# Optimization experiments

Measured on AMD Instinct MI355X. Metric: run time of the kernel, lower is better.

Reference implementation:

```python
import jax, jax.numpy as jnp
import numpy as np

DIM = 768
HEADS = 12
DIM_HEAD = 64
INNER = HEADS * DIM_HEAD  # 768
SCALE = DIM_HEAD ** -0.5


def setup_inputs() -> dict:
    key = jax.random.key(0)
    k1, k2, k3, k4 = jax.random.split(key, 4)
    b, n = 8, 1024
    x = jax.random.normal(k1, (b, n, DIM), dtype=jnp.float32)
    # fused QKV projection, no bias: y = x @ w_qkv  -> [b, n, 3*inner]
    w_qkv = jax.random.normal(k2, (DIM, 3 * INNER), dtype=jnp.float32) * (DIM ** -0.5)
    # output projection with bias
    w_out = jax.random.normal(k3, (INNER, DIM), dtype=jnp.float32) * (INNER ** -0.5)
    b_out = jax.random.normal(k4, (DIM,), dtype=jnp.float32) * 0.02
    return {"x": x, "w_qkv": w_qkv, "w_out": w_out, "b_out": b_out}


def reference(x, w_qkv, w_out, b_out):
    b, n, _ = x.shape
    qkv = jnp.einsum('bnd,de->bne', x, w_qkv)  # [b, n, 3*inner]
    q, k, v = jnp.split(qkv, 3, axis=-1)
    # 'b n (h d) -> b h n d'
    def split_heads(t):
        return t.reshape(b, n, HEADS, DIM_HEAD).transpose(0, 2, 1, 3)
    q, k, v = split_heads(q), split_heads(k), split_heads(v)
    dots = jnp.einsum('bhid,bhjd->bhij', q, k) * SCALE  # [b, h, n, n]
    attn = jax.nn.softmax(dots, axis=-1)
    out = jnp.einsum('bhij,bhjd->bhid', attn, v)  # [b, h, n, d]
    out = out.transpose(0, 2, 1, 3).reshape(b, n, INNER)  # 'b h n d -> b n (h d)'
    return jnp.einsum('bne,ed->bnd', out, w_out) + b_out
```

## Files before the change

### kernel.cpp

```cpp
#include <hip/hip_runtime.h>

typedef unsigned short u16;
typedef __bf16 bf16x8 __attribute__((ext_vector_type(8)));
typedef float f32x4 __attribute__((ext_vector_type(4)));

__device__ inline u16 f2bf(float f) {
    union { float f; unsigned int u; } a; a.f = f;
    unsigned int u = a.u + 0x7fffu + ((a.u >> 16) & 1u);
    return (u16)(u >> 16);
}
__device__ __forceinline__ float truncbf(float f, u16& h) {
    union { float f; unsigned int u; } a; a.f = f;
    a.u &= 0xffff0000u;
    h = (u16)(a.u >> 16);
    return a.f;
}

__device__ __forceinline__ void cp16(const void* g, void* l) {
    __builtin_amdgcn_global_load_lds(
        (const __attribute__((address_space(1))) unsigned int*)g,
        (__attribute__((address_space(3))) unsigned int*)l, 16, 0, 0);
}

__global__ __launch_bounds__(256) void prep(
    const float* __restrict__ x, const float* __restrict__ wq,
    const float* __restrict__ wo, u16* __restrict__ xbf,
    u16* __restrict__ wtq, u16* __restrict__ wto)
{
    int bid = blockIdx.x;
    if (bid < 3072) {
        size_t base = ((size_t)bid * 256 + threadIdx.x) * 8;
        float4 f0 = *(const float4*)&x[base];
        float4 f1 = *(const float4*)&x[base + 4];
        union { u16 s[8]; uint4 v; } t;
        t.s[0]=f2bf(f0.x); t.s[1]=f2bf(f0.y); t.s[2]=f2bf(f0.z); t.s[3]=f2bf(f0.w);
        t.s[4]=f2bf(f1.x); t.s[5]=f2bf(f1.y); t.s[6]=f2bf(f1.z); t.s[7]=f2bf(f1.w);
        *(uint4*)&xbf[base] = t.v;
        return;
    }
    __shared__ u16 tile[32][33];
    const float* in; u16* outp; int N, bx, by;
    if (bid < 3072 + 1728) { int t = bid - 3072; in = wq; outp = wtq; N = 2304; bx = t % 72; by = t / 72; }
    else                   { int t = bid - 4800; in = wo; outp = wto; N = 768;  bx = t % 24; by = t / 24; }
    int n0 = bx * 32, k0 = by * 32;
    int tx = threadIdx.x & 31, ty = threadIdx.x >> 5;
    #pragma unroll
    for (int r = ty; r < 32; r += 8)
        tile[r][tx] = f2bf(in[(size_t)(k0 + r) * N + n0 + tx]);
    __syncthreads();
    #pragma unroll
    for (int r = ty; r < 32; r += 8)
        outp[(size_t)(n0 + r) * 768 + k0 + tx] = tile[tx][r];
}

__global__ __launch_bounds__(256) void gemm_qkv(
    const u16* __restrict__ A, const u16* __restrict__ Bt,
    u16* __restrict__ q_out, u16* __restrict__ k_out, u16* __restrict__ v_out)
{
    const int K = 768;
    __shared__ __align__(16) u16 As[128 * 64];
    __shared__ __align__(16) u16 Bs[128 * 64];

    int tid = threadIdx.x;
    int lane = tid & 63, wave = tid >> 6;
    int quad = lane >> 4, l16 = lane & 15;
    int wm = wave >> 1, wn = wave & 1;
    int id = blockIdx.x;
    int xcd = id & 7, j = id >> 3;
    int m0 = (((j & 7) << 3) + xcd) * 128;
    int n0 = (j >> 3) * 128;

    f32x4 acc[4][4];
    #pragma unroll
    for (int i = 0; i < 4; i++)
        #pragma unroll
        for (int jj = 0; jj < 4; jj++) acc[i][jj] = (f32x4){0.f, 0.f, 0.f, 0.f};

    int r0 = tid >> 3, cg = tid & 7;
    for (int kt = 0; kt < K; kt += 64) {
        #pragma unroll
        for (int it = 0; it < 4; ++it) {
            int row = it * 32 + r0;
            int g = cg ^ (row & 7);
            cp16(&A [(size_t)(m0 + row) * K + kt + g * 8], &As[(size_t)(it * 256 + tid) * 8]);
            cp16(&Bt[(size_t)(n0 + row) * K + kt + g * 8], &Bs[(size_t)(it * 256 + tid) * 8]);
        }
        __syncthreads();
        #pragma unroll
        for (int ko = 0; ko < 2; ko++) {
            bf16x8 af[4], bfr[4];
            #pragma unroll
            for (int i = 0; i < 4; i++) {
                int R = wm * 64 + i * 16 + l16;
                af[i] = *(const bf16x8*)&As[R * 64 + (((ko * 4 + quad) ^ (R & 7)) * 8)];
            }
            #pragma unroll
            for (int jj = 0; jj < 4; jj++) {
                int R = wn * 64 + jj * 16 + l16;
                bfr[jj] = *(const bf16x8*)&Bs[R * 64 + (((ko * 4 + quad) ^ (R & 7)) * 8)];
            }
            #pragma unroll
            for (int i = 0; i < 4; i++)
                #pragma unroll
                for (int jj = 0; jj < 4; jj++)
                    acc[i][jj] = __builtin_amdgcn_mfma_f32_16x16x32_bf16(af[i], bfr[jj], acc[i][jj], 0, 0, 0);
        }
        __syncthreads();
    }

    int M0 = m0 + wm * 64, N0 = n0 + wn * 64;
    int part = N0 >= 1536 ? 2 : (N0 >= 768 ? 1 : 0);
    int h = (N0 - part * 768) >> 6;
    int b = M0 >> 10, npos0 = M0 & 1023;
    u16* ep = (wave < 2 ? As : Bs) + (wave & 1) * 4096;

    if (part != 2) {
        float scale = (part == 0) ? 0.18033688011112042f : 1.0f;
        u16* gbase = (part == 0 ? q_out : k_out) + (((size_t)(b * 12 + h) * 1024 + npos0) << 6);
        #pragma unroll
        for (int i = 0; i < 4; i++)
            #pragma unroll
            for (int jj = 0; jj < 4; jj++) {
                int dd = jj * 16 + l16;
                #pragma unroll
                for (int r = 0; r < 4; r++) {
                    int np = i * 16 + quad * 4 + r;
                    ep[np * 64 + (((dd >> 3) ^ (np & 7)) * 8) + (dd & 7)] =
                        f2bf(acc[i][jj][r] * scale);
                }
            }
        __syncthreads();
        #pragma unroll
        for (int t = 0; t < 8; t++) {
            int idx = t * 512 + lane * 8;
            int np = idx >> 6;
            int slot = ((lane & 7) ^ (np & 7));
            uint4 v = *(const uint4*)&ep[np * 64 + slot * 8];
            *(uint4*)&gbase[idx] = v;
        }
    } else {
        #pragma unroll
        for (int i = 0; i < 4; i++)
            #pragma unroll
            for (int jj = 0; jj < 4; jj++) {
                int dd = jj * 16 + l16;
                int npg = i * 2 + (quad >> 1);
                int sub = (quad & 1) * 4;
                union { u16 s[4]; uint2 v; } pk;
                #pragma unroll
                for (int r = 0; r < 4; r++) pk.s[r] = f2bf(acc[i][jj][r]);
                *(uint2*)&ep[dd * 64 + ((npg ^ (dd & 7)) * 8) + sub] = pk.v;
            }
        __syncthreads();
        #pragma unroll
        for (int t = 0; t < 8; t++) {
            int dd = t * 8 + (lane >> 3);
            int npg = lane & 7;
            uint4 v = *(const uint4*)&ep[dd * 64 + ((npg ^ (dd & 7)) * 8)];
            *(uint4*)&v_out[((size_t)((b * 12 + h) * 64 + dd)) * 1024 + npos0 + npg * 8] = v;
        }
    }
}

__global__ __launch_bounds__(256) void attn128(
    u16* __restrict__ QO, const u16* __restrict__ Kg, const u16* __restrict__ Vtg)
{
    __shared__ __align__(16) u16 Ks[64 * 64];
    __shared__ __align__(16) u16 Vs[64 * 64];

    int tid = threadIdx.x;
    int lane = tid & 63, wave = tid >> 6;
    int quad = lane >> 4, l16 = lane & 15;
    int id = blockIdx.x;
    int xcd = id & 7, j = id >> 3;
    int bh = xcd * 12 + (j >> 3);
    int q0 = (j & 7) * 128;
    const size_t head_base = (size_t)bh * 65536;

    size_t qoff[2];
    bf16x8 qf[2][2];
    #pragma unroll
    for (int qs = 0; qs < 2; qs++) {
        qoff[qs] = head_base + (size_t)(q0 + wave * 32 + qs * 16 + l16) * 64;
        qf[qs][0] = *(const bf16x8*)&QO[qoff[qs] + quad * 8];
        qf[qs][1] = *(const bf16x8*)&QO[qoff[qs] + 32 + quad * 8];
    }

    f32x4 Oacc[4][2];
    #pragma unroll
    for (int dt = 0; dt < 4; dt++)
        #pragma unroll
        for (int qs = 0; qs < 2; qs++) Oacc[dt][qs] = (f32x4){0.f, 0.f, 0.f, 0.f};
    float l_part[2] = {0.f, 0.f};

    int srow = tid >> 3, sg = tid & 7;
    for (int j0 = 0; j0 < 1024; j0 += 64) {
        #pragma unroll
        for (int it = 0; it < 2; ++it) {
            int e = it * 256 + tid, row = it * 32 + srow, gs = sg ^ (row & 7);
            cp16(&Kg [head_base + (size_t)(j0 + row) * 64 + gs * 8], &Ks[(size_t)e * 8]);
            cp16(&Vtg[head_base + (size_t)row * 1024 + j0 + gs * 8], &Vs[(size_t)e * 8]);
        }
        __syncthreads();

        f32x4 s4[4][2];
        #pragma unroll
        for (int nt = 0; nt < 4; nt++) {
            int R = nt * 16 + l16;
            bf16x8 kf0 = *(const bf16x8*)&Ks[R * 64 + ((quad       ^ (R & 7)) * 8)];
            bf16x8 kf1 = *(const bf16x8*)&Ks[R * 64 + (((quad + 4) ^ (R & 7)) * 8)];
            #pragma unroll
            for (int qs = 0; qs < 2; qs++) {
                f32x4 s = (f32x4){0.f, 0.f, 0.f, 0.f};
                s = __builtin_amdgcn_mfma_f32_16x16x32_bf16(kf0, qf[qs][0], s, 0, 0, 0);
                s = __builtin_amdgcn_mfma_f32_16x16x32_bf16(kf1, qf[qs][1], s, 0, 0, 0);
                s4[nt][qs] = s;
            }
        }

        u16 ph[4][2][4];
        #pragma unroll
        for (int nt = 0; nt < 4; nt++)
            #pragma unroll
            for (int qs = 0; qs < 2; qs++)
                #pragma unroll
                for (int r = 0; r < 4; r++) {
                    float p = __builtin_amdgcn_exp2f(s4[nt][qs][r]);
                    l_part[qs] += truncbf(p, ph[nt][qs][r]);
                }

        #pragma unroll
        for (int h = 0; h < 2; h++) {
            union { u16 s[8]; bf16x8 v; } pk[2];
            #pragma unroll
            for (int qs = 0; qs < 2; qs++)
                #pragma unroll
                for (int r = 0; r < 4; r++) {
                    pk[qs].s[r]     = ph[2 * h][qs][r];
                    pk[qs].s[4 + r] = ph[2 * h + 1][qs][r];
                }
            int lg0 = 4 * h + (quad >> 1), lg1 = lg0 + 2;
            int off = (quad & 1) * 4;
            #pragma unroll
            for (int dt = 0; dt < 4; dt++) {
                int drow = dt * 16 + l16;
                union { u16 s[8]; bf16x8 v; } vk;
                *(uint2*)&vk.s[0] = *(const uint2*)&Vs[drow * 64 + (lg0 ^ (drow & 7)) * 8 + off];
                *(uint2*)&vk.s[4] = *(const uint2*)&Vs[drow * 64 + (lg1 ^ (drow & 7)) * 8 + off];
                #pragma unroll
                for (int qs = 0; qs < 2; qs++)
                    Oacc[dt][qs] = __builtin_amdgcn_mfma_f32_16x16x32_bf16(vk.v, pk[qs].v, Oacc[dt][qs], 0, 0, 0);
            }
        }
        __syncthreads();
    }

    #pragma unroll
    for (int qs = 0; qs < 2; qs++) {
        float l = l_part[qs];
        l += __shfl_xor(l, 16);
        l += __shfl_xor(l, 32);
        float rl = __builtin_amdgcn_rcpf(l);
        #pragma unroll
        for (int dt = 0; dt < 4; dt++) {
            union { u16 s[4]; uint2 v; } ok;
            #pragma unroll
            for (int r = 0; r < 4; r++) ok.s[r] = f2bf(Oacc[dt][qs][r] * rl);
            *(uint2*)&QO[qoff[qs] + dt * 16 + quad * 4] = ok.v;
        }
    }
}

__global__ __launch_bounds__(256) void gemm_out(
    const u16* __restrict__ Qg, const u16* __restrict__ Bt,
    const float* __restrict__ bias, float* __restrict__ out)
{
    const int K = 768;
    __shared__ __align__(16) u16 As[128 * 64];
    __shared__ __align__(16) u16 Bs[128 * 64];

    int tid = threadIdx.x;
    int lane = tid & 63, wave = tid >> 6;
    int quad = lane >> 4, l16 = lane & 15;
    int wm = wave >> 1, wn = wave & 1;
    int id = blockIdx.x;
    int xcd = id & 7, j = id >> 3;
    int m0 = (((j & 7) << 3) + xcd) * 128;
    int n0 = (j >> 3) * 128;

    f32x4 acc[4][4];
    #pragma unroll
    for (int i = 0; i < 4; i++)
        #pragma unroll
        for (int jj = 0; jj < 4; jj++) acc[i][jj] = (f32x4){0.f, 0.f, 0.f, 0.f};

    int r0 = tid >> 3, cg = tid & 7;
    for (int kt = 0; kt < K; kt += 64) {
        int h = kt >> 6;
        #pragma unroll
        for (int it = 0; it < 4; ++it) {
            int row = it * 32 + r0;
            int g = cg ^ (row & 7);
            int m = m0 + row, b = m >> 10, npos = m & 1023;
            cp16(&Qg[(((size_t)(b * 12 + h) * 1024 + npos) << 6) + g * 8],
                 &As[(size_t)(it * 256 + tid) * 8]);
            cp16(&Bt[(size_t)(n0 + row) * K + kt + g * 8],
                 &Bs[(size_t)(it * 256 + tid) * 8]);
        }
        __syncthreads();
        #pragma unroll
        for (int ko = 0; ko < 2; ko++) {
            bf16x8 af[4], bfr[4];
            #pragma unroll
            for (int i = 0; i < 4; i++) {
                int R = wm * 64 + i * 16 + l16;
                af[i] = *(const bf16x8*)&As[R * 64 + (((ko * 4 + quad) ^ (R & 7)) * 8)];
            }
            #pragma unroll
            for (int jj = 0; jj < 4; jj++) {
                int R = wn * 64 + jj * 16 + l16;
                bfr[jj] = *(const bf16x8*)&Bs[R * 64 + (((ko * 4 + quad) ^ (R & 7)) * 8)];
            }
            #pragma unroll
            for (int i = 0; i < 4; i++)
                #pragma unroll
                for (int jj = 0; jj < 4; jj++)
                    acc[i][jj] = __builtin_amdgcn_mfma_f32_16x16x32_bf16(af[i], bfr[jj], acc[i][jj], 0, 0, 0);
        }
        __syncthreads();
    }

    #pragma unroll
    for (int i = 0; i < 4; i++) {
        int mbase = m0 + wm * 64 + i * 16 + quad * 4;
        #pragma unroll
        for (int jj = 0; jj < 4; jj++) {
            int n = n0 + wn * 64 + jj * 16 + l16;
            float bv = bias[n];
            #pragma unroll
            for (int r = 0; r < 4; r++)
                out[(size_t)(mbase + r) * 768 + n] = acc[i][jj][r] + bv;
        }
    }
}

extern "C" void kernel_launch(void* const* d_in, const int* in_sizes, int n_in,
                              void* d_out, int out_size, void* d_ws, size_t ws_size,
                              hipStream_t stream) {
    const float* x     = (const float*)d_in[0];
    const float* w_qkv = (const float*)d_in[1];
    const float* w_out = (const float*)d_in[2];
    const float* b_out = (const float*)d_in[3];
    float* out = (float*)d_out;

    char* ws = (char*)d_ws;
    u16* wtq  = (u16*)(ws);
    u16* wto  = (u16*)(ws + 3538944);
    u16* Qbuf = (u16*)(ws + 4718592);
    u16* xbf  = (u16*)(ws + 17301504);
    u16* Kbuf = (u16*)d_out;
    u16* Vbuf = (u16*)d_out + 6291456;

    prep<<<dim3(5376), 256, 0, stream>>>(x, w_qkv, w_out, xbf, wtq, wto);
    gemm_qkv<<<dim3(1152), 256, 0, stream>>>(xbf, wtq, Qbuf, Kbuf, Vbuf);
    attn128<<<dim3(768), 256, 0, stream>>>(Qbuf, Kbuf, Vbuf);
    gemm_out<<<dim3(384), 256, 0, stream>>>(Qbuf, wto, b_out, out);
}
```

Measured before the change: 194.3 us.

## Double-buffer LDS tiles with async prefetch in GEMM and attention kernels

All three main kernels (QKV GEMM, attention, output GEMM) now keep two LDS buffers. Each iteration issues async global-to-LDS loads for the next K/V or K-tile into the other buffer while it runs MFMAs on the current one. Fragments are read into registers before the prefetch is issued, which lets each loop drop to a single barrier per iteration. Global address pointers are precomputed outside the loops, and the redundant epilogue barriers in the QKV GEMM are removed. The cost is doubled LDS use per block, which may lower occupancy, plus more registers for the held fragments.

```diff
diff --git a/kernel.cpp b/kernel.cpp
--- a/kernel.cpp
+++ b/kernel.cpp
@@ -58,8 +58,8 @@
     u16* __restrict__ q_out, u16* __restrict__ k_out, u16* __restrict__ v_out)
 {
     const int K = 768;
-    __shared__ __align__(16) u16 As[128 * 64];
-    __shared__ __align__(16) u16 Bs[128 * 64];
+    __shared__ __align__(16) u16 As[2][128 * 64];
+    __shared__ __align__(16) u16 Bs[2][128 * 64];
 
     int tid = threadIdx.x;
     int lane = tid & 63, wave = tid >> 6;
@@ -77,46 +77,55 @@
         for (int jj = 0; jj < 4; jj++) acc[i][jj] = (f32x4){0.f, 0.f, 0.f, 0.f};
 
     int r0 = tid >> 3, cg = tid & 7;
-    for (int kt = 0; kt < K; kt += 64) {
-        #pragma unroll
-        for (int it = 0; it < 4; ++it) {
-            int row = it * 32 + r0;
-            int g = cg ^ (row & 7);
-            cp16(&A [(size_t)(m0 + row) * K + kt + g * 8], &As[(size_t)(it * 256 + tid) * 8]);
-            cp16(&Bt[(size_t)(n0 + row) * K + kt + g * 8], &Bs[(size_t)(it * 256 + tid) * 8]);
-        }
+    int g = cg ^ (r0 & 7);
+    const u16* GA[4]; const u16* GB[4];
+    #pragma unroll
+    for (int it = 0; it < 4; it++) {
+        GA[it] = A  + (size_t)(m0 + it * 32 + r0) * K + g * 8;
+        GB[it] = Bt + (size_t)(n0 + it * 32 + r0) * K + g * 8;
+    }
+
+    #define STAGE_QKV(kt, b)                                          \
+        _Pragma("unroll")                                             \
+        for (int it = 0; it < 4; it++) {                              \
+            cp16(GA[it] + (kt), &As[b][(it * 256 + tid) * 8]);        \
+            cp16(GB[it] + (kt), &Bs[b][(it * 256 + tid) * 8]);        \
+        }
+
+    STAGE_QKV(0, 0)
+    for (int i = 0; i < 12; i++) {
+        int b = i & 1;
         __syncthreads();
-        #pragma unroll
-        for (int ko = 0; ko < 2; ko++) {
-            bf16x8 af[4], bfr[4];
-            #pragma unroll
-            for (int i = 0; i < 4; i++) {
-                int R = wm * 64 + i * 16 + l16;
-                af[i] = *(const bf16x8*)&As[R * 64 + (((ko * 4 + quad) ^ (R & 7)) * 8)];
-            }
-            #pragma unroll
-            for (int jj = 0; jj < 4; jj++) {
-                int R = wn * 64 + jj * 16 + l16;
-                bfr[jj] = *(const bf16x8*)&Bs[R * 64 + (((ko * 4 + quad) ^ (R & 7)) * 8)];
-            }
-            #pragma unroll
-            for (int i = 0; i < 4; i++)
-                #pragma unroll
-                for (int jj = 0; jj < 4; jj++)
-                    acc[i][jj] = __builtin_amdgcn_mfma_f32_16x16x32_bf16(af[i], bfr[jj], acc[i][jj], 0, 0, 0);
-        }
-        __syncthreads();
-    }
+        bf16x8 af[2][4], bfr[2][4];
+        #pragma unroll
+        for (int ko = 0; ko < 2; ko++)
+            #pragma unroll
+            for (int x = 0; x < 4; x++) {
+                int Ra = wm * 64 + x * 16 + l16;
+                af[ko][x]  = *(const bf16x8*)&As[b][Ra * 64 + (((ko * 4 + quad) ^ (Ra & 7)) * 8)];
+                int Rb = wn * 64 + x * 16 + l16;
+                bfr[ko][x] = *(const bf16x8*)&Bs[b][Rb * 64 + (((ko * 4 + quad) ^ (Rb & 7)) * 8)];
+            }
+        if (i + 1 < 12) { STAGE_QKV((i + 1) * 64, b ^ 1) }
+        #pragma unroll
+        for (int ko = 0; ko < 2; ko++)
+            #pragma unroll
+            for (int x = 0; x < 4; x++)
+                #pragma unroll
+                for (int y = 0; y < 4; y++)
+                    acc[x][y] = __builtin_amdgcn_mfma_f32_16x16x32_bf16(af[ko][x], bfr[ko][y], acc[x][y], 0, 0, 0);
+    }
+    #undef STAGE_QKV
 
     int M0 = m0 + wm * 64, N0 = n0 + wn * 64;
     int part = N0 >= 1536 ? 2 : (N0 >= 768 ? 1 : 0);
     int h = (N0 - part * 768) >> 6;
-    int b = M0 >> 10, npos0 = M0 & 1023;
-    u16* ep = (wave < 2 ? As : Bs) + (wave & 1) * 4096;
+    int b2 = M0 >> 10, npos0 = M0 & 1023;
+    u16* ep = (wave < 2 ? As[0] : Bs[0]) + (wave & 1) * 4096;
 
     if (part != 2) {
         float scale = (part == 0) ? 0.18033688011112042f : 1.0f;
-        u16* gbase = (part == 0 ? q_out : k_out) + (((size_t)(b * 12 + h) * 1024 + npos0) << 6);
+        u16* gbase = (part == 0 ? q_out : k_out) + (((size_t)(b2 * 12 + h) * 1024 + npos0) << 6);
         #pragma unroll
         for (int i = 0; i < 4; i++)
             #pragma unroll
@@ -129,7 +138,6 @@
                         f2bf(acc[i][jj][r] * scale);
                 }
             }
-        __syncthreads();
         #pragma unroll
         for (int t = 0; t < 8; t++) {
             int idx = t * 512 + lane * 8;
@@ -151,13 +159,12 @@
                 for (int r = 0; r < 4; r++) pk.s[r] = f2bf(acc[i][jj][r]);
                 *(uint2*)&ep[dd * 64 + ((npg ^ (dd & 7)) * 8) + sub] = pk.v;
             }
-        __syncthreads();
         #pragma unroll
         for (int t = 0; t < 8; t++) {
             int dd = t * 8 + (lane >> 3);
             int npg = lane & 7;
             uint4 v = *(const uint4*)&ep[dd * 64 + ((npg ^ (dd & 7)) * 8)];
-            *(uint4*)&v_out[((size_t)((b * 12 + h) * 64 + dd)) * 1024 + npos0 + npg * 8] = v;
+            *(uint4*)&v_out[((size_t)((b2 * 12 + h) * 64 + dd)) * 1024 + npos0 + npg * 8] = v;
         }
     }
 }
@@ -165,8 +172,8 @@
 __global__ __launch_bounds__(256) void attn128(
     u16* __restrict__ QO, const u16* __restrict__ Kg, const u16* __restrict__ Vtg)
 {
-    __shared__ __align__(16) u16 Ks[64 * 64];
-    __shared__ __align__(16) u16 Vs[64 * 64];
+    __shared__ __align__(16) u16 Ks[2][64 * 64];
+    __shared__ __align__(16) u16 Vs[2][64 * 64];
 
     int tid = threadIdx.x;
     int lane = tid & 63, wave = tid >> 6;
@@ -194,29 +201,44 @@
     float l_part[2] = {0.f, 0.f};
 
     int srow = tid >> 3, sg = tid & 7;
-    for (int j0 = 0; j0 < 1024; j0 += 64) {
-        #pragma unroll
-        for (int it = 0; it < 2; ++it) {
-            int e = it * 256 + tid, row = it * 32 + srow, gs = sg ^ (row & 7);
-            cp16(&Kg [head_base + (size_t)(j0 + row) * 64 + gs * 8], &Ks[(size_t)e * 8]);
-            cp16(&Vtg[head_base + (size_t)row * 1024 + j0 + gs * 8], &Vs[(size_t)e * 8]);
-        }
+    int gs = sg ^ (srow & 7);
+    const u16* GK[2]; const u16* GV[2];
+    #pragma unroll
+    for (int it = 0; it < 2; it++) {
+        GK[it] = Kg  + head_base + (size_t)(it * 32 + srow) * 64 + gs * 8;
+        GV[it] = Vtg + head_base + (size_t)(it * 32 + srow) * 1024 + gs * 8;
+    }
+
+    #define STAGE_ATT(j0, b)                                          \
+        _Pragma("unroll")                                             \
+        for (int it = 0; it < 2; it++) {                              \
+            cp16(GK[it] + (size_t)(j0) * 64, &Ks[b][(it * 256 + tid) * 8]); \
+            cp16(GV[it] + (j0),             &Vs[b][(it * 256 + tid) * 8]); \
+        }
+
+    STAGE_ATT(0, 0)
+    for (int i = 0; i < 16; i++) {
+        int b = i & 1;
         __syncthreads();
-
-        f32x4 s4[4][2];
+        bf16x8 kf[4][2];
         #pragma unroll
         for (int nt = 0; nt < 4; nt++) {
             int R = nt * 16 + l16;
-            bf16x8 kf0 = *(const bf16x8*)&Ks[R * 64 + ((quad       ^ (R & 7)) * 8)];
-            bf16x8 kf1 = *(const bf16x8*)&Ks[R * 64 + (((quad + 4) ^ (R & 7)) * 8)];
+            kf[nt][0] = *(const bf16x8*)&Ks[b][R * 64 + ((quad       ^ (R & 7)) * 8)];
+            kf[nt][1] = *(const bf16x8*)&Ks[b][R * 64 + (((quad + 4) ^ (R & 7)) * 8)];
+        }
+        if (i + 1 < 16) { STAGE_ATT((i + 1) * 64, b ^ 1) }
+
+        f32x4 s4[4][2];
+        #pragma unroll
+        for (int nt = 0; nt < 4; nt++)
             #pragma unroll
             for (int qs = 0; qs < 2; qs++) {
                 f32x4 s = (f32x4){0.f, 0.f, 0.f, 0.f};
-                s = __builtin_amdgcn_mfma_f32_16x16x32_bf16(kf0, qf[qs][0], s, 0, 0, 0);
-                s = __builtin_amdgcn_mfma_f32_16x16x32_bf16(kf1, qf[qs][1], s, 0, 0, 0);
+                s = __builtin_amdgcn_mfma_f32_16x16x32_bf16(kf[nt][0], qf[qs][0], s, 0, 0, 0);
+                s = __builtin_amdgcn_mfma_f32_16x16x32_bf16(kf[nt][1], qf[qs][1], s, 0, 0, 0);
                 s4[nt][qs] = s;
             }
-        }
 
         u16 ph[4][2][4];
         #pragma unroll
@@ -245,15 +267,15 @@
             for (int dt = 0; dt < 4; dt++) {
                 int drow = dt * 16 + l16;
                 union { u16 s[8]; bf16x8 v; } vk;
-                *(uint2*)&vk.s[0] = *(const uint2*)&Vs[drow * 64 + (lg0 ^ (drow & 7)) * 8 + off];
-                *(uint2*)&vk.s[4] = *(const uint2*)&Vs[drow * 64 + (lg1 ^ (drow & 7)) * 8 + off];
+                *(uint2*)&vk.s[0] = *(const uint2*)&Vs[b][drow * 64 + (lg0 ^ (drow & 7)) * 8 + off];
+                *(uint2*)&vk.s[4] = *(const uint2*)&Vs[b][drow * 64 + (lg1 ^ (drow & 7)) * 8 + off];
                 #pragma unroll
                 for (int qs = 0; qs < 2; qs++)
                     Oacc[dt][qs] = __builtin_amdgcn_mfma_f32_16x16x32_bf16(vk.v, pk[qs].v, Oacc[dt][qs], 0, 0, 0);
             }
         }
-        __syncthreads();
-    }
+    }
+    #undef STAGE_ATT
 
     #pragma unroll
     for (int qs = 0; qs < 2; qs++) {
@@ -276,8 +298,8 @@
     const float* __restrict__ bias, float* __restrict__ out)
 {
     const int K = 768;
-    __shared__ __align__(16) u16 As[128 * 64];
-    __shared__ __align__(16) u16 Bs[128 * 64];
+    __shared__ __align__(16) u16 As[2][128 * 64];
+    __shared__ __align__(16) u16 Bs[2][128 * 64];
 
     int tid = threadIdx.x;
     int lane = tid & 63, wave = tid >> 6;
@@ -295,40 +317,46 @@
         for (int jj = 0; jj < 4; jj++) acc[i][jj] = (f32x4){0.f, 0.f, 0.f, 0.f};
 
     int r0 = tid >> 3, cg = tid & 7;
-    for (int kt = 0; kt < K; kt += 64) {
-        int h = kt >> 6;
-        #pragma unroll
-        for (int it = 0; it < 4; ++it) {
-            int row = it * 32 + r0;
-            int g = cg ^ (row & 7);
-            int m = m0 + row, b = m >> 10, npos = m & 1023;
-            cp16(&Qg[(((size_t)(b * 12 + h) * 1024 + npos) << 6) + g * 8],
-                 &As[(size_t)(it * 256 + tid) * 8]);
-            cp16(&Bt[(size_t)(n0 + row) * K + kt + g * 8],
-                 &Bs[(size_t)(it * 256 + tid) * 8]);
-        }
+    int g = cg ^ (r0 & 7);
+    const u16* GA[4]; const u16* GB[4];
+    #pragma unroll
+    for (int it = 0; it < 4; it++) {
+        int m = m0 + it * 32 + r0, b = m >> 10, npos = m & 1023;
+        GA[it] = Qg + (((size_t)(b * 12) * 1024 + npos) << 6) + g * 8;
+        GB[it] = Bt + (size_t)(n0 + it * 32 + r0) * K + g * 8;
+    }
+
+    #define STAGE_OUT(i2, b)                                              \
+        _Pragma("unroll")                                                 \
+        for (int it = 0; it < 4; it++) {                                  \
+            cp16(GA[it] + (size_t)(i2) * 65536, &As[b][(it * 256 + tid) * 8]); \
+            cp16(GB[it] + (i2) * 64,            &Bs[b][(it * 256 + tid) * 8]); \
+        }
+
+    STAGE_OUT(0, 0)
+    for (int i = 0; i < 12; i++) {
+        int b = i & 1;
         __syncthreads();
-        #pragma unroll
-        for (int ko = 0; ko < 2; ko++) {
-            bf16x8 af[4], bfr[4];
-            #pragma unroll
-            for (int i = 0; i < 4; i++) {
-                int R = wm * 64 + i * 16 + l16;
-                af[i] = *(const bf16x8*)&As[R * 64 + (((ko * 4 + quad) ^ (R & 7)) * 8)];
-            }
-            #pragma unroll
-            for (int jj = 0; jj < 4; jj++) {
-                int R = wn * 64 + jj * 16 + l16;
-                bfr[jj] = *(const bf16x8*)&Bs[R * 64 + (((ko * 4 + quad) ^ (R & 7)) * 8)];
-            }
-            #pragma unroll
-            for (int i = 0; i < 4; i++)
-                #pragma unroll
-                for (int jj = 0; jj < 4; jj++)
-                    acc[i][jj] = __builtin_amdgcn_mfma_f32_16x16x32_bf16(af[i], bfr[jj], acc[i][jj], 0, 0, 0);
-        }
-        __syncthreads();
-    }
+        bf16x8 af[2][4], bfr[2][4];
+        #pragma unroll
+        for (int ko = 0; ko < 2; ko++)
+            #pragma unroll
+            for (int x = 0; x < 4; x++) {
+                int Ra = wm * 64 + x * 16 + l16;
+                af[ko][x]  = *(const bf16x8*)&As[b][Ra * 64 + (((ko * 4 + quad) ^ (Ra & 7)) * 8)];
+                int Rb = wn * 64 + x * 16 + l16;
+                bfr[ko][x] = *(const bf16x8*)&Bs[b][Rb * 64 + (((ko * 4 + quad) ^ (Rb & 7)) * 8)];
+            }
+        if (i + 1 < 12) { STAGE_OUT(i + 1, b ^ 1) }
+        #pragma unroll
+        for (int ko = 0; ko < 2; ko++)
+            #pragma unroll
+            for (int x = 0; x < 4; x++)
+                #pragma unroll
+                for (int y = 0; y < 4; y++)
+                    acc[x][y] = __builtin_amdgcn_mfma_f32_16x16x32_bf16(af[ko][x], bfr[ko][y], acc[x][y], 0, 0, 0);
+    }
+    #undef STAGE_OUT
 
     #pragma unroll
     for (int i = 0; i < 4; i++) {
```

After: 183.7 us. 5.5% less time.
